# Kernel tuning notes

Hardware: AMD Instinct MI355X
Metric: run time of the kernel (lower is better)

The kernel has to match this reference:

```python
import jax, jax.numpy as jnp
import numpy as np

HIDDEN = 20


def setup_inputs() -> dict:
    key = jax.random.key(0)
    ks = jax.random.split(key, 8)
    B, T = 8192, 2048
    x = jax.random.normal(ks[0], (B, T), dtype=jnp.float32)
    # linear1: 1 -> HIDDEN
    W1 = jax.random.normal(ks[1], (HIDDEN, 1), dtype=jnp.float32) * 0.5
    b1 = jax.random.normal(ks[2], (HIDDEN,), dtype=jnp.float32) * 0.1
    # LSTMCell(HIDDEN, HIDDEN): torch layout [4*H, H], gate order i,f,g,o
    W_ih = jax.random.normal(ks[3], (4 * HIDDEN, HIDDEN), dtype=jnp.float32) * 0.2
    W_hh = jax.random.normal(ks[4], (4 * HIDDEN, HIDDEN), dtype=jnp.float32) * 0.2
    b_ih = jax.random.normal(ks[5], (4 * HIDDEN,), dtype=jnp.float32) * 0.1
    b_hh = jax.random.normal(ks[6], (4 * HIDDEN,), dtype=jnp.float32) * 0.1
    # linear2: HIDDEN -> 1
    W2 = jax.random.normal(ks[7], (1, HIDDEN), dtype=jnp.float32) * 0.2
    b2 = jnp.zeros((1,), dtype=jnp.float32)
    return {"input": x, "W1": W1, "b1": b1, "W_ih": W_ih, "W_hh": W_hh,
            "b_ih": b_ih, "b_hh": b_hh, "W2": W2, "b2": b2}


def reference(input, W1, b1, W_ih, W_hh, b_ih, b_hh, W2, b2):
    B, T = input.shape
    h0 = jnp.zeros((B, HIDDEN), dtype=input.dtype)
    c0 = jnp.zeros((B, HIDDEN), dtype=input.dtype)

    def step(carry, x_t):
        h, c = carry
        # linear1 on scalar input: [B] -> [B, HIDDEN]
        hid = x_t[:, None] * W1[:, 0][None, :] + b1
        # LSTMCell gates, torch order: i, f, g, o
        gates = hid @ W_ih.T + b_ih + h @ W_hh.T + b_hh  # [B, 4H]
        i_g, f_g, g_g, o_g = jnp.split(gates, 4, axis=-1)
        c_new = jax.nn.sigmoid(f_g) * c + jax.nn.sigmoid(i_g) * jnp.tanh(g_g)
        h_new = jax.nn.sigmoid(o_g) * jnp.tanh(c_new)
        out = h_new @ W2.T + b2  # [B, 1]
        return (h_new, c_new), out[:, 0]

    xs = input.T  # [T, B]
    _, outs = jax.lax.scan(step, (h0, c0), xs)  # outs: [T, B]
    return outs.T  # [B, T]
```

## Files before the change

### kernel.cpp

```cpp
#include <hip/hip_runtime.h>


#define HID 20
#define ROWS_PER_WAVE 3
#define NTHREADS 64
#define L2E 1.4426950408889634f

typedef float v2f __attribute__((ext_vector_type(2)));

__device__ __forceinline__ float exp2_hw(float v) { return __builtin_amdgcn_exp2f(v); }
__device__ __forceinline__ float rcp_hw(float v)  { return __builtin_amdgcn_rcpf(v); }

__device__ __forceinline__ float sig_s(float gs) {
    return rcp_hw(1.0f + exp2_hw(-gs));
}
__device__ __forceinline__ float tanh_2Ls(float gs2) {
    return (2.0f * L2E) - (4.0f * L2E) * rcp_hw(1.0f + exp2_hw(gs2));
}
__device__ __forceinline__ float tanh_c(float cs) {
    return 1.0f - 2.0f * rcp_hw(1.0f + exp2_hw(cs));
}

__global__ __attribute__((amdgpu_flat_work_group_size(NTHREADS, NTHREADS),
                          amdgpu_waves_per_eu(3, 3)))
void lstm_wave(
        const float* __restrict__ x,
        const float* __restrict__ W1,
        const float* __restrict__ b1,
        const float* __restrict__ W_ih,
        const float* __restrict__ W_hh,
        const float* __restrict__ b_ih,
        const float* __restrict__ b_hh,
        const float* __restrict__ W2,
        const float* __restrict__ b2,
        float* __restrict__ out,
        const int B, const int T)
{
    const int lane = threadIdx.x;
    const int lrow = lane / HID;
    const int m    = lane % HID;
    const bool outlane = (lrow == 3) && (m < ROWS_PER_WAVE);
    const int rslot = (lrow == 3) ? m : lrow;
    const long rowbase = (long)blockIdx.x * ROWS_PER_WAVE;
    const long row = rowbase + ((lrow == 3) ? (long)((m < 3) ? m : 0) : (long)lrow);
    const long arow = (row < B) ? row : (B - 1);
    const bool ovalid = outlane && (row < B);

    __shared__ __align__(16) float hbuf[ROWS_PER_WAVE + 1][HID];

    float u[4], v[4];
    if (lrow < 3) {
#pragma unroll
        for (int g = 0; g < 4; ++g) {
            const int j = g * HID + m;
            const float s = (g == 2) ? (2.0f * L2E) : L2E;
            float uu = 0.f, vv = 0.f;
#pragma unroll
            for (int k = 0; k < HID; ++k) {
                const float wi = W_ih[j * HID + k];
                uu += wi * W1[k];
                vv += wi * b1[k];
            }
            u[g] = s * uu;
            v[g] = s * (vv + b_ih[j] + b_hh[j]);
        }
    } else {
#pragma unroll
        for (int g = 0; g < 4; ++g) { u[g] = 0.f; v[g] = 0.f; }
        v[0] = b2[0];
    }

    v2f whh2[4][HID / 2];
    if (lrow < 3) {
#pragma unroll
        for (int g = 0; g < 4; ++g) {
            const int j = g * HID + m;
            const float s = (g == 2) ? (2.0f * L2E) : L2E;
#pragma unroll
            for (int kk = 0; kk < HID / 2; ++kk) {
                v2f w;
                w.x = s * W_hh[j * HID + 2 * kk];
                w.y = s * W_hh[j * HID + 2 * kk + 1];
                whh2[g][kk] = w;
            }
        }
    } else {
#pragma unroll
        for (int kk = 0; kk < HID / 2; ++kk) {
            v2f w; w.x = W2[2 * kk]; w.y = W2[2 * kk + 1];
            whh2[0][kk] = w;
            whh2[1][kk] = (v2f)(0.f);
            whh2[2][kk] = (v2f)(0.f);
            whh2[3][kk] = (v2f)(0.f);
        }
    }

#pragma unroll
    for (int g = 0; g < 4; ++g)
#pragma unroll
        for (int kk = 0; kk < HID / 2; ++kk)
            asm volatile("" : "+v"(whh2[g][kk]));

    float cs = 0.f;
    hbuf[lrow][m] = 0.f;
    if (lane < HID) hbuf[3][lane] = 0.f;

    const float* __restrict__ xrow = x   + arow * T;
    float* __restrict__       orow = out + arow * T;

    const float4* __restrict__ rdp = (const float4*)&hbuf[rslot][0];
    float* __restrict__        wrp = &hbuf[lrow][m];

    float4 F0 = rdp[0], F1 = rdp[1], F2 = rdp[2], F3 = rdp[3], F4 = rdp[4];

    float4 xq = *(const float4*)&xrow[0];
    float4 xq_next;
    float4 obuf = make_float4(0.f, 0.f, 0.f, 0.f);

#define FQ(Q, FF)                                                               \
    {   v2f hA; hA.x = (FF).x; hA.y = (FF).y;                                   \
        v2f hB; hB.x = (FF).z; hB.y = (FF).w;                                   \
        a0 = __builtin_elementwise_fma(whh2[0][2*Q],   hA, a0);                 \
        a1 = __builtin_elementwise_fma(whh2[1][2*Q],   hA, a1);                 \
        a2 = __builtin_elementwise_fma(whh2[2][2*Q],   hA, a2);                 \
        a3 = __builtin_elementwise_fma(whh2[3][2*Q],   hA, a3);                 \
        a0 = __builtin_elementwise_fma(whh2[0][2*Q+1], hB, a0);                 \
        a1 = __builtin_elementwise_fma(whh2[1][2*Q+1], hB, a1);                 \
        a2 = __builtin_elementwise_fma(whh2[2][2*Q+1], hB, a2);                 \
        a3 = __builtin_elementwise_fma(whh2[3][2*Q+1], hB, a3);                 }

#define BODY(XV, OSLOT)                                                         \
    {                                                                           \
        const float xv = (XV);                                                  \
        v2f a0, a1, a2, a3;                                                     \
        a0.x = v[0] + xv * u[0]; a0.y = 0.f;                                    \
        a1.x = v[1] + xv * u[1]; a1.y = 0.f;                                    \
        a2.x = v[2] + xv * u[2]; a2.y = 0.f;                                    \
        a3.x = v[3] + xv * u[3]; a3.y = 0.f;                                    \
        FQ(0, F0) FQ(1, F1) FQ(2, F2) FQ(3, F3) FQ(4, F4)                       \
        const float g0 = a0.x + a0.y;                                           \
        const float g1 = a1.x + a1.y;                                           \
        const float g2 = a2.x + a2.y;                                           \
        const float g3 = a3.x + a3.y;                                           \
        OSLOT = g0;                                                             \
        const float ig  = sig_s(g0);                                            \
        const float fg  = sig_s(g1);                                            \
        const float ggs = tanh_2Ls(g2);                                         \
        const float og  = sig_s(g3);                                            \
        cs = fg * cs + ig * ggs;                                                \
        *wrp = og * tanh_c(cs);                                                 \
        F0 = rdp[0]; F1 = rdp[1]; F2 = rdp[2]; F3 = rdp[3]; F4 = rdp[4];        \
    }

    for (int t = 0; t < T; t += 4) {
        const int tp = (t + 4 < T) ? (t + 4) : t;
        xq_next = *(const float4*)&xrow[tp];

        BODY(xq.x, obuf.w)
        if (t >= 4 && ovalid) *(float4*)&orow[t - 4] = obuf;
        BODY(xq.y, obuf.x)
        BODY(xq.z, obuf.y)
        BODY(xq.w, obuf.z)

        xq = xq_next;
    }

    {
        float o = v[0];
        o += whh2[0][0].x * F0.x + whh2[0][0].y * F0.y
           + whh2[0][1].x * F0.z + whh2[0][1].y * F0.w;
        o += whh2[0][2].x * F1.x + whh2[0][2].y * F1.y
           + whh2[0][3].x * F1.z + whh2[0][3].y * F1.w;
        o += whh2[0][4].x * F2.x + whh2[0][4].y * F2.y
           + whh2[0][5].x * F2.z + whh2[0][5].y * F2.w;
        o += whh2[0][6].x * F3.x + whh2[0][6].y * F3.y
           + whh2[0][7].x * F3.z + whh2[0][7].y * F3.w;
        o += whh2[0][8].x * F4.x + whh2[0][8].y * F4.y
           + whh2[0][9].x * F4.z + whh2[0][9].y * F4.w;
        obuf.w = o;
        if (ovalid) *(float4*)&orow[T - 4] = obuf;
    }
#undef BODY
#undef FQ
}

extern "C" void kernel_launch(void* const* d_in, const int* in_sizes, int n_in,
                              void* d_out, int out_size, void* d_ws, size_t ws_size,
                              hipStream_t stream) {
    (void)n_in; (void)d_ws; (void)ws_size; (void)out_size;
    const float* x    = (const float*)d_in[0];
    const float* W1   = (const float*)d_in[1];
    const float* b1   = (const float*)d_in[2];
    const float* W_ih = (const float*)d_in[3];
    const float* W_hh = (const float*)d_in[4];
    const float* b_ih = (const float*)d_in[5];
    const float* b_hh = (const float*)d_in[6];
    const float* W2   = (const float*)d_in[7];
    const float* b2   = (const float*)d_in[8];
    float* out        = (float*)d_out;

    const int B = 8192;
    const int T = in_sizes[0] / B;
    const int grid = (B + ROWS_PER_WAVE - 1) / ROWS_PER_WAVE;

    lstm_wave<<<grid, NTHREADS, 0, stream>>>(x, W1, b1, W_ih, W_hh, b_ih, b_hh, W2, b2, out, B, T);
}
```

Baseline: 1.077 ms.

## Interleave two independent LSTM row streams per wave to hide latency

Each wave now processes two independent groups of three batch rows, interleaving their timestep bodies so that the LDS round-trip and transcendental latency of one stream can overlap with compute of the other. This halves the grid size and lowers the occupancy target from three to two waves per EU to make room for the doubled state registers. The gain relies on instruction-level parallelism inside a wave replacing the latency hiding previously provided by more resident waves. The risk is register pressure or spills, and fewer waves to switch between.

```diff
diff --git a/kernel.cpp b/kernel.cpp
--- a/kernel.cpp
+++ b/kernel.cpp
@@ -2,7 +2,8 @@
 
 
 #define HID 20
-#define ROWS_PER_WAVE 3
+#define ROWS_PER_STREAM 3
+#define ROWS_PER_BLOCK 6
 #define NTHREADS 64
 #define L2E 1.4426950408889634f
 
@@ -22,7 +23,7 @@
 }
 
 __global__ __attribute__((amdgpu_flat_work_group_size(NTHREADS, NTHREADS),
-                          amdgpu_waves_per_eu(3, 3)))
+                          amdgpu_waves_per_eu(2, 2)))
 void lstm_wave(
         const float* __restrict__ x,
         const float* __restrict__ W1,
@@ -39,14 +40,17 @@
     const int lane = threadIdx.x;
     const int lrow = lane / HID;
     const int m    = lane % HID;
-    const bool outlane = (lrow == 3) && (m < ROWS_PER_WAVE);
+    const bool outlane = (lrow == 3) && (m < ROWS_PER_STREAM);
     const int rslot = (lrow == 3) ? m : lrow;
-    const long rowbase = (long)blockIdx.x * ROWS_PER_WAVE;
-    const long row = rowbase + ((lrow == 3) ? (long)((m < 3) ? m : 0) : (long)lrow);
-    const long arow = (row < B) ? row : (B - 1);
-    const bool ovalid = outlane && (row < B);
-
-    __shared__ __align__(16) float hbuf[ROWS_PER_WAVE + 1][HID];
+    const long rowbase = (long)blockIdx.x * ROWS_PER_BLOCK;
+    const long rowA = rowbase + ((lrow == 3) ? (long)((m < 3) ? m : 0) : (long)lrow);
+    const long rowB = rowA + ROWS_PER_STREAM;
+    const long arowA = (rowA < B) ? rowA : (B - 1);
+    const long arowB = (rowB < B) ? rowB : (B - 1);
+    const bool ovalidA = outlane && (rowA < B);
+    const bool ovalidB = outlane && (rowB < B);
+
+    __shared__ __align__(16) float hbuf[2][ROWS_PER_STREAM + 1][HID];
 
     float u[4], v[4];
     if (lrow < 3) {
@@ -101,21 +105,29 @@
         for (int kk = 0; kk < HID / 2; ++kk)
             asm volatile("" : "+v"(whh2[g][kk]));
 
-    float cs = 0.f;
-    hbuf[lrow][m] = 0.f;
-    if (lane < HID) hbuf[3][lane] = 0.f;
-
-    const float* __restrict__ xrow = x   + arow * T;
-    float* __restrict__       orow = out + arow * T;
-
-    const float4* __restrict__ rdp = (const float4*)&hbuf[rslot][0];
-    float* __restrict__        wrp = &hbuf[lrow][m];
-
-    float4 F0 = rdp[0], F1 = rdp[1], F2 = rdp[2], F3 = rdp[3], F4 = rdp[4];
-
-    float4 xq = *(const float4*)&xrow[0];
-    float4 xq_next;
-    float4 obuf = make_float4(0.f, 0.f, 0.f, 0.f);
+    float csA = 0.f, csB = 0.f;
+    hbuf[0][lrow][m] = 0.f;
+    hbuf[1][lrow][m] = 0.f;
+    if (lane < HID) { hbuf[0][3][lane] = 0.f; hbuf[1][3][lane] = 0.f; }
+
+    const float* __restrict__ xrowA = x   + arowA * T;
+    const float* __restrict__ xrowB = x   + arowB * T;
+    float* __restrict__       orowA = out + arowA * T;
+    float* __restrict__       orowB = out + arowB * T;
+
+    const float4* __restrict__ rdpA = (const float4*)&hbuf[0][rslot][0];
+    const float4* __restrict__ rdpB = (const float4*)&hbuf[1][rslot][0];
+    float* __restrict__        wrpA = &hbuf[0][lrow][m];
+    float* __restrict__        wrpB = &hbuf[1][lrow][m];
+
+    float4 FA0 = rdpA[0], FA1 = rdpA[1], FA2 = rdpA[2], FA3 = rdpA[3], FA4 = rdpA[4];
+    float4 FB0 = rdpB[0], FB1 = rdpB[1], FB2 = rdpB[2], FB3 = rdpB[3], FB4 = rdpB[4];
+
+    float4 xqA = *(const float4*)&xrowA[0];
+    float4 xqB = *(const float4*)&xrowB[0];
+    float4 xqA_next, xqB_next;
+    float4 obufA = make_float4(0.f, 0.f, 0.f, 0.f);
+    float4 obufB = make_float4(0.f, 0.f, 0.f, 0.f);
 
 #define FQ(Q, FF)                                                               \
     {   v2f hA; hA.x = (FF).x; hA.y = (FF).y;                                   \
@@ -129,7 +141,7 @@
         a2 = __builtin_elementwise_fma(whh2[2][2*Q+1], hB, a2);                 \
         a3 = __builtin_elementwise_fma(whh2[3][2*Q+1], hB, a3);                 }
 
-#define BODY(XV, OSLOT)                                                         \
+#define BODY(CS, WRP, RDP, F0, F1, F2, F3, F4, XV, OSLOT)                       \
     {                                                                           \
         const float xv = (XV);                                                  \
         v2f a0, a1, a2, a3;                                                     \
@@ -147,39 +159,57 @@
         const float fg  = sig_s(g1);                                            \
         const float ggs = tanh_2Ls(g2);                                         \
         const float og  = sig_s(g3);                                            \
-        cs = fg * cs + ig * ggs;                                                \
-        *wrp = og * tanh_c(cs);                                                 \
-        F0 = rdp[0]; F1 = rdp[1]; F2 = rdp[2]; F3 = rdp[3]; F4 = rdp[4];        \
-    }
+        CS = fg * CS + ig * ggs;                                                \
+        *(WRP) = og * tanh_c(CS);                                               \
+        F0 = (RDP)[0]; F1 = (RDP)[1]; F2 = (RDP)[2];                            \
+        F3 = (RDP)[3]; F4 = (RDP)[4];                                           \
+    }
+
+#define BODYA(XV, OSLOT) BODY(csA, wrpA, rdpA, FA0, FA1, FA2, FA3, FA4, XV, OSLOT)
+#define BODYB(XV, OSLOT) BODY(csB, wrpB, rdpB, FB0, FB1, FB2, FB3, FB4, XV, OSLOT)
 
     for (int t = 0; t < T; t += 4) {
         const int tp = (t + 4 < T) ? (t + 4) : t;
-        xq_next = *(const float4*)&xrow[tp];
-
-        BODY(xq.x, obuf.w)
-        if (t >= 4 && ovalid) *(float4*)&orow[t - 4] = obuf;
-        BODY(xq.y, obuf.x)
-        BODY(xq.z, obuf.y)
-        BODY(xq.w, obuf.z)
-
-        xq = xq_next;
-    }
-
-    {
-        float o = v[0];
-        o += whh2[0][0].x * F0.x + whh2[0][0].y * F0.y
-           + whh2[0][1].x * F0.z + whh2[0][1].y * F0.w;
-        o += whh2[0][2].x * F1.x + whh2[0][2].y * F1.y
-           + whh2[0][3].x * F1.z + whh2[0][3].y * F1.w;
-        o += whh2[0][4].x * F2.x + whh2[0][4].y * F2.y
-           + whh2[0][5].x * F2.z + whh2[0][5].y * F2.w;
-        o += whh2[0][6].x * F3.x + whh2[0][6].y * F3.y
-           + whh2[0][7].x * F3.z + whh2[0][7].y * F3.w;
-        o += whh2[0][8].x * F4.x + whh2[0][8].y * F4.y
-           + whh2[0][9].x * F4.z + whh2[0][9].y * F4.w;
-        obuf.w = o;
-        if (ovalid) *(float4*)&orow[T - 4] = obuf;
-    }
+        xqA_next = *(const float4*)&xrowA[tp];
+        xqB_next = *(const float4*)&xrowB[tp];
+
+        BODYA(xqA.x, obufA.w)
+        if (t >= 4 && ovalidA) *(float4*)&orowA[t - 4] = obufA;
+        BODYB(xqB.x, obufB.w)
+        if (t >= 4 && ovalidB) *(float4*)&orowB[t - 4] = obufB;
+        BODYA(xqA.y, obufA.x)
+        BODYB(xqB.y, obufB.x)
+        BODYA(xqA.z, obufA.y)
+        BODYB(xqB.z, obufB.y)
+        BODYA(xqA.w, obufA.z)
+        BODYB(xqB.w, obufB.z)
+
+        xqA = xqA_next;
+        xqB = xqB_next;
+    }
+
+#define EPILOG(F0, F1, F2, F3, F4, OBUF, OVALID, OROW)                          \
+    {                                                                           \
+        float o = v[0];                                                         \
+        o += whh2[0][0].x * (F0).x + whh2[0][0].y * (F0).y                      \
+           + whh2[0][1].x * (F0).z + whh2[0][1].y * (F0).w;                     \
+        o += whh2[0][2].x * (F1).x + whh2[0][2].y * (F1).y                      \
+           + whh2[0][3].x * (F1).z + whh2[0][3].y * (F1).w;                     \
+        o += whh2[0][4].x * (F2).x + whh2[0][4].y * (F2).y                      \
+           + whh2[0][5].x * (F2).z + whh2[0][5].y * (F2).w;                     \
+        o += whh2[0][6].x * (F3).x + whh2[0][6].y * (F3).y                      \
+           + whh2[0][7].x * (F3).z + whh2[0][7].y * (F3).w;                     \
+        o += whh2[0][8].x * (F4).x + whh2[0][8].y * (F4).y                      \
+           + whh2[0][9].x * (F4).z + whh2[0][9].y * (F4).w;                     \
+        (OBUF).w = o;                                                           \
+        if (OVALID) *(float4*)&(OROW)[T - 4] = (OBUF);                          \
+    }
+
+    EPILOG(FA0, FA1, FA2, FA3, FA4, obufA, ovalidA, orowA)
+    EPILOG(FB0, FB1, FB2, FB3, FB4, obufB, ovalidB, orowB)
+#undef EPILOG
+#undef BODYA
+#undef BODYB
 #undef BODY
 #undef FQ
 }
@@ -201,7 +231,7 @@
 
     const int B = 8192;
     const int T = in_sizes[0] / B;
-    const int grid = (B + ROWS_PER_WAVE - 1) / ROWS_PER_WAVE;
+    const int grid = (B + ROWS_PER_BLOCK - 1) / ROWS_PER_BLOCK;
 
     lstm_wave<<<grid, NTHREADS, 0, stream>>>(x, W1, b1, W_ih, W_hh, b_ih, b_hh, W2, b2, out, B, T);
 }
```

Measured after the change: 1.446 ms. 34.3% more time.
